# Performance work log

Measured on AMD Instinct MI355X. Metric: run time of the kernel, lower is better.

Reference implementation:

```python
import jax, jax.numpy as jnp
import numpy as np

B = 131072
D = 64
H1 = 512
H2 = 256
NC = 128  # nurse classes
DC = 128  # doctor classes
EPS = 1e-5
NEG = -1e9


def _kaiming(key, fan_in, fan_out):
    # kaiming_normal_ with mode='fan_out', relu gain: std = sqrt(2/fan_out)
    return jax.random.normal(key, (fan_in, fan_out), jnp.float32) * jnp.sqrt(2.0 / fan_out)


def setup_inputs() -> dict:
    key = jax.random.key(0)
    ks = jax.random.split(key, 16)
    x = jax.random.normal(ks[0], (B, D), jnp.float32)
    sn = jax.random.randint(ks[1], (B,), 0, NC)
    sd = jax.random.randint(ks[2], (B,), 0, DC)
    # last-4 / last-3 columns carry the per-sample max class thresholds
    x = x.at[:, -4].set(sn.astype(jnp.float32)).at[:, -3].set(sd.astype(jnp.float32))
    inp = {
        'x': x,
        'W0': _kaiming(ks[3], D, H1), 'b0': jnp.zeros((H1,), jnp.float32),
        'g0': jnp.ones((H1,), jnp.float32), 'be0': jnp.zeros((H1,), jnp.float32),
        'rm0': jax.random.normal(ks[4], (H1,), jnp.float32) * 0.1,
        'rv0': jax.random.uniform(ks[5], (H1,), jnp.float32, 0.5, 1.5),
        'W1': _kaiming(ks[6], H1, H2), 'b1': jnp.zeros((H2,), jnp.float32),
        'g1': jnp.ones((H2,), jnp.float32), 'be1': jnp.zeros((H2,), jnp.float32),
        'rm1': jax.random.normal(ks[7], (H2,), jnp.float32) * 0.1,
        'rv1': jax.random.uniform(ks[8], (H2,), jnp.float32, 0.5, 1.5),
        'nW1': _kaiming(ks[9], H2, 64), 'nb1': jnp.zeros((64,), jnp.float32),
        'nW2': _kaiming(ks[10], 64, NC), 'nb2': jnp.zeros((NC,), jnp.float32),
        'dW1': _kaiming(ks[11], H2, 64), 'db1': jnp.zeros((64,), jnp.float32),
        'dW2': _kaiming(ks[12], 64, DC), 'db2': jnp.zeros((DC,), jnp.float32),
    }
    return inp


def _bn(h, g, be, rm, rv):
    # BatchNorm1d inference: normalize with running stats
    return (h - rm) * (g * jax.lax.rsqrt(rv + EPS)) + be


def reference(x, W0, b0, g0, be0, rm0, rv0, W1, b1, g1, be1, rm1, rv1,
              nW1, nb1, nW2, nb2, dW1, db1, dW2, db2):
    s_nurse = x[:, -4].astype(jnp.int32)   # [B]
    s_doctor = x[:, -3].astype(jnp.int32)  # [B]

    h = jax.nn.relu(_bn(x @ W0 + b0, g0, be0, rm0, rv0))   # [B,H1]
    h = jax.nn.relu(_bn(h @ W1 + b1, g1, be1, rm1, rv1))   # [B,H2]

    nurse_logits = jax.nn.relu(h @ nW1 + nb1) @ nW2 + nb2   # [B,NC]
    doctor_logits = jax.nn.relu(h @ dW1 + db1) @ dW2 + db2  # [B,DC]

    # vectorized range mask: positions <= s_max are kept
    nmask = (jnp.arange(NC)[None, :] <= s_nurse[:, None]).astype(nurse_logits.dtype)
    dmask = (jnp.arange(DC)[None, :] <= s_doctor[:, None]).astype(doctor_logits.dtype)
    nurse_logits = nurse_logits * nmask + (1.0 - nmask) * NEG
    doctor_logits = doctor_logits * dmask + (1.0 - dmask) * NEG
    return (nurse_logits, doctor_logits)
```

## Files before the change

kernel.cpp:

```cpp
#include <hip/hip_runtime.h>

#define NB 131072
#define NEG9 -1e9f

typedef __attribute__((ext_vector_type(8))) __bf16 bf16x8;
typedef __attribute__((ext_vector_type(4))) float f32x4;
typedef __attribute__((ext_vector_type(2))) unsigned int u32x2;
typedef __attribute__((ext_vector_type(4))) unsigned int u32x4;

__device__ __forceinline__ f32x4 mfma16(bf16x8 a, bf16x8 b, f32x4 c) {
    return __builtin_amdgcn_mfma_f32_16x16x32_bf16(a, b, c, 0, 0, 0);
}

__device__ __forceinline__ unsigned pk(float h, float l) {
    return __builtin_amdgcn_perm(__builtin_bit_cast(unsigned, h),
                                 __builtin_bit_cast(unsigned, l), 0x07060302u);
}
__device__ __forceinline__ unsigned pku(unsigned h, unsigned l) {
    return __builtin_amdgcn_perm(h, l, 0x07060302u);
}

__device__ __forceinline__ unsigned short f2bf(float f) {
    unsigned u = __builtin_bit_cast(unsigned, f);
    u += 0x7fffu + ((u >> 16) & 1u);
    return (unsigned short)(u >> 16);
}

struct __align__(16) Wspace {
    unsigned short W0t[512][64];
    unsigned short W1t[256][512];
    unsigned short nW1t[64][256];
    unsigned short dW1t[64][256];
    unsigned short nW2t[128][64];
    unsigned short dW2t[128][64];
    float c0[512];
    float c1[256];
    float nb1c[64], db1c[64];
    float nb2c[128], db2c[128];
};

__device__ Wspace g_ws;

__global__ __launch_bounds__(256) void prep_kernel(
    const float* __restrict__ W0, const float* __restrict__ b0,
    const float* __restrict__ g0, const float* __restrict__ be0,
    const float* __restrict__ rm0, const float* __restrict__ rv0,
    const float* __restrict__ W1, const float* __restrict__ b1,
    const float* __restrict__ g1, const float* __restrict__ be1,
    const float* __restrict__ rm1, const float* __restrict__ rv1,
    const float* __restrict__ nW1, const float* __restrict__ nb1,
    const float* __restrict__ nW2, const float* __restrict__ nb2,
    const float* __restrict__ dW1, const float* __restrict__ db1,
    const float* __restrict__ dW2, const float* __restrict__ db2)
{
    const int b = blockIdx.x;
    const int t = threadIdx.x;

    if (b == 52) {
        {
            int i = t;          g_ws.c0[i] = (b0[i] - rm0[i]) * (g0[i] * rsqrtf(rv0[i] + 1e-5f)) + be0[i];
            i = t + 256;        g_ws.c0[i] = (b0[i] - rm0[i]) * (g0[i] * rsqrtf(rv0[i] + 1e-5f)) + be0[i];
        }
        g_ws.c1[t] = (b1[t] - rm1[t]) * (g1[t] * rsqrtf(rv1[t] + 1e-5f)) + be1[t];
        if (t < 64)  { g_ws.nb1c[t] = nb1[t]; g_ws.db1c[t] = db1[t]; }
        if (t < 128) { g_ws.nb2c[t] = nb2[t]; g_ws.db2c[t] = db2[t]; }
        return;
    }

    const float* src; unsigned short* dst;
    const float* gp = nullptr; const float* rvp = nullptr;
    int sld, dld, k0, n0;
    if (b < 32)      { src = W1;  dst = (unsigned short*)g_ws.W1t;  sld = 256; dld = 512;
                       k0 = (b >> 2) * 64; n0 = (b & 3) * 64; gp = g1; rvp = rv1; }
    else if (b < 40) { src = W0;  dst = (unsigned short*)g_ws.W0t;  sld = 512; dld = 64;
                       k0 = 0; n0 = (b - 32) * 64; gp = g0; rvp = rv0; }
    else if (b < 44) { src = nW1; dst = (unsigned short*)g_ws.nW1t; sld = 64;  dld = 256;
                       k0 = (b - 40) * 64; n0 = 0; }
    else if (b < 48) { src = dW1; dst = (unsigned short*)g_ws.dW1t; sld = 64;  dld = 256;
                       k0 = (b - 44) * 64; n0 = 0; }
    else if (b < 50) { src = nW2; dst = (unsigned short*)g_ws.nW2t; sld = 128; dld = 64;
                       k0 = 0; n0 = (b - 48) * 64; }
    else             { src = dW2; dst = (unsigned short*)g_ws.dW2t; sld = 128; dld = 64;
                       k0 = 0; n0 = (b - 50) * 64; }

    __shared__ unsigned short tile[64][66];

    const int rr = t >> 4;
    const int cc = (t & 15) * 4;

#pragma unroll
    for (int g = 0; g < 4; ++g) {
        const int r = rr + g * 16;
        f32x4 v = *(const f32x4*)&src[(size_t)(k0 + r) * sld + n0 + cc];
        if (gp) {
            f32x4 gv = *(const f32x4*)&gp[n0 + cc];
            f32x4 rv = *(const f32x4*)&rvp[n0 + cc];
            v[0] *= gv[0] * rsqrtf(rv[0] + 1e-5f);
            v[1] *= gv[1] * rsqrtf(rv[1] + 1e-5f);
            v[2] *= gv[2] * rsqrtf(rv[2] + 1e-5f);
            v[3] *= gv[3] * rsqrtf(rv[3] + 1e-5f);
        }
        *(unsigned*)&tile[r][cc]     = (unsigned)f2bf(v[0]) | ((unsigned)f2bf(v[1]) << 16);
        *(unsigned*)&tile[r][cc + 2] = (unsigned)f2bf(v[2]) | ((unsigned)f2bf(v[3]) << 16);
    }
    __syncthreads();

#pragma unroll
    for (int g = 0; g < 4; ++g) {
        const int n = rr + g * 16;
        unsigned o01 = (unsigned)tile[cc + 0][n] | ((unsigned)tile[cc + 1][n] << 16);
        unsigned o23 = (unsigned)tile[cc + 2][n] | ((unsigned)tile[cc + 3][n] << 16);
        u32x2 o = { o01, o23 };
        *(u32x2*)&dst[(size_t)(n0 + n) * dld + k0 + cc] = o;
    }
}

__global__ __launch_bounds__(512, 4) void fused_mlp(
    const u32x4* __restrict__ xu, float* __restrict__ out)
{
    __shared__ __align__(16) unsigned short sXs[8 * 64 * 8];
    __shared__ __align__(16) unsigned short sH0[64 * 64 * 8];

    const int tid = threadIdx.x;
    const int w = tid >> 6;
    const int lane = tid & 63;
    const int m = lane & 15;
    const int q = lane >> 4;
    const int qh = q >> 1;
    const int ql = (q & 1) * 4;
    const int row0 = blockIdx.x * 64;

    {
        int r = tid >> 3, g = tid & 7;
        u32x4 v0 = __builtin_nontemporal_load(&xu[(size_t)(row0 + r) * 16 + g * 2]);
        u32x4 v1 = __builtin_nontemporal_load(&xu[(size_t)(row0 + r) * 16 + g * 2 + 1]);
        u32x4 p = { pku(v0[1], v0[0]), pku(v0[3], v0[2]), pku(v1[1], v1[0]), pku(v1[3], v1[2]) };
        *(u32x4*)&sXs[(g * 64 + r) * 8] = p;
    }
    __syncthreads();

    bf16x8 xr[2][4];
#pragma unroll
    for (int g2 = 0; g2 < 2; ++g2)
#pragma unroll
        for (int mt = 0; mt < 4; ++mt)
            xr[g2][mt] = *(const bf16x8*)&sXs[((g2 * 4 + q) * 64 + mt * 16 + m) * 8];

#pragma unroll
    for (int nt = 0; nt < 4; ++nt) {
        const int gcb = w * 64 + nt * 16;
        bf16x8 wa0 = *(const bf16x8*)&g_ws.W0t[gcb + m][q * 8];
        bf16x8 wa1 = *(const bf16x8*)&g_ws.W0t[gcb + m][32 + q * 8];
        f32x4 bias = *(const f32x4*)&g_ws.c0[gcb + q * 4];
        const int kg = w * 8 + nt * 2 + qh;
#pragma unroll
        for (int mt = 0; mt < 4; ++mt) {
            f32x4 c = {0.f, 0.f, 0.f, 0.f};
            c = mfma16(wa0, xr[0][mt], c);
            c = mfma16(wa1, xr[1][mt], c);
            u32x2 pw = { pk(fmaxf(c[1] + bias[1], 0.f), fmaxf(c[0] + bias[0], 0.f)),
                         pk(fmaxf(c[3] + bias[3], 0.f), fmaxf(c[2] + bias[2], 0.f)) };
            *(u32x2*)&sH0[(kg * 64 + mt * 16 + m) * 8 + ql] = pw;
        }
    }
    __syncthreads();

    f32x4 acc1[2][4];
#pragma unroll
    for (int a = 0; a < 2; ++a)
#pragma unroll
        for (int b = 0; b < 4; ++b) acc1[a][b] = f32x4{0.f, 0.f, 0.f, 0.f};

#pragma unroll
    for (int ks = 0; ks < 16; ++ks) {
        bf16x8 wb[2], ab[4];
#pragma unroll
        for (int nt = 0; nt < 2; ++nt)
            wb[nt] = *(const bf16x8*)&g_ws.W1t[w * 32 + nt * 16 + m][ks * 32 + q * 8];
#pragma unroll
        for (int mt = 0; mt < 4; ++mt)
            ab[mt] = *(const bf16x8*)&sH0[((ks * 4 + q) * 64 + mt * 16 + m) * 8];
#pragma unroll
        for (int nt = 0; nt < 2; ++nt)
#pragma unroll
            for (int mt = 0; mt < 4; ++mt)
                acc1[nt][mt] = mfma16(wb[nt], ab[mt], acc1[nt][mt]);
    }
    __syncthreads();

#pragma unroll
    for (int nt = 0; nt < 2; ++nt) {
        const int cb = w * 32 + nt * 16;
        f32x4 bias = *(const f32x4*)&g_ws.c1[cb + q * 4];
        const int kg = w * 4 + nt * 2 + qh;
#pragma unroll
        for (int mt = 0; mt < 4; ++mt) {
            f32x4 c = acc1[nt][mt];
            u32x2 pw = { pk(fmaxf(c[1] + bias[1], 0.f), fmaxf(c[0] + bias[0], 0.f)),
                         pk(fmaxf(c[3] + bias[3], 0.f), fmaxf(c[2] + bias[2], 0.f)) };
            *(u32x2*)&sH0[(kg * 64 + mt * 16 + m) * 8 + ql] = pw;
        }
    }
    __syncthreads();

    const int head = w >> 2;
    {
        const int cb = (w & 3) * 16;
        const unsigned short (*Wh)[256] = head ? g_ws.dW1t : g_ws.nW1t;
        const float* bh = head ? g_ws.db1c : g_ws.nb1c;
        f32x4 acc[4];
#pragma unroll
        for (int b = 0; b < 4; ++b) acc[b] = f32x4{0.f, 0.f, 0.f, 0.f};
#pragma unroll
        for (int ks = 0; ks < 8; ++ks) {
            bf16x8 wh = *(const bf16x8*)&Wh[cb + m][ks * 32 + q * 8];
#pragma unroll
            for (int mt = 0; mt < 4; ++mt) {
                bf16x8 ab = *(const bf16x8*)&sH0[((ks * 4 + q) * 64 + mt * 16 + m) * 8];
                acc[mt] = mfma16(wh, ab, acc[mt]);
            }
        }
        __syncthreads();
        unsigned short* Ah = sH0 + (head ? 4096 : 0);
        f32x4 bias = *(const f32x4*)&bh[cb + q * 4];
        const int kg = (w & 3) * 2 + qh;
#pragma unroll
        for (int mt = 0; mt < 4; ++mt) {
            f32x4 c = acc[mt];
            u32x2 pw = { pk(fmaxf(c[1] + bias[1], 0.f), fmaxf(c[0] + bias[0], 0.f)),
                         pk(fmaxf(c[3] + bias[3], 0.f), fmaxf(c[2] + bias[2], 0.f)) };
            *(u32x2*)&Ah[(kg * 64 + mt * 16 + m) * 8 + ql] = pw;
        }
    }
    __syncthreads();

    {
        const unsigned short (*W2)[64] = head ? g_ws.dW2t : g_ws.nW2t;
        const float* b2 = head ? g_ws.db2c : g_ws.nb2c;
        const unsigned short* Ah = sH0 + (head ? 4096 : 0);
        float* op = out + (size_t)head * (size_t)NB * 128;

        int thr[4];
#pragma unroll
        for (int mt = 0; mt < 4; ++mt) {
            unsigned tv = *(const unsigned*)&sXs[(7 * 64 + mt * 16 + m) * 8 + 4];
            thr[mt] = (int)__builtin_bit_cast(float, head ? (tv & 0xffff0000u) : (tv << 16));
        }
#pragma unroll
        for (int ct = 0; ct < 2; ++ct) {
            const int ocb = (w & 3) * 32 + ct * 16;
            bf16x8 w0 = *(const bf16x8*)&W2[ocb + m][q * 8];
            bf16x8 w1 = *(const bf16x8*)&W2[ocb + m][32 + q * 8];
            f32x4 bias = *(const f32x4*)&b2[ocb + q * 4];
#pragma unroll
            for (int mt = 0; mt < 4; ++mt) {
                bf16x8 a0 = *(const bf16x8*)&Ah[(q * 64 + mt * 16 + m) * 8];
                bf16x8 a1 = *(const bf16x8*)&Ah[((4 + q) * 64 + mt * 16 + m) * 8];
                f32x4 c = {0.f, 0.f, 0.f, 0.f};
                c = mfma16(w0, a0, c);
                c = mfma16(w1, a1, c);
                const int ci = ocb + q * 4;
                const int t = thr[mt];
                f32x4 v;
                v[0] = (ci + 0 <= t) ? c[0] + bias[0] : NEG9;
                v[1] = (ci + 1 <= t) ? c[1] + bias[1] : NEG9;
                v[2] = (ci + 2 <= t) ? c[2] + bias[2] : NEG9;
                v[3] = (ci + 3 <= t) ? c[3] + bias[3] : NEG9;
                *(f32x4*)&op[(size_t)(row0 + mt * 16 + m) * 128 + ci] = v;
            }
        }
    }
}

extern "C" void kernel_launch(void* const* d_in, const int* in_sizes, int n_in,
                              void* d_out, int out_size, void* d_ws, size_t ws_size,
                              hipStream_t stream) {
    (void)in_sizes; (void)n_in; (void)d_ws; (void)ws_size;

    prep_kernel<<<53, 256, 0, stream>>>(
        (const float*)d_in[1], (const float*)d_in[2], (const float*)d_in[3],
        (const float*)d_in[4], (const float*)d_in[5], (const float*)d_in[6],
        (const float*)d_in[7], (const float*)d_in[8], (const float*)d_in[9],
        (const float*)d_in[10], (const float*)d_in[11], (const float*)d_in[12],
        (const float*)d_in[13], (const float*)d_in[14], (const float*)d_in[15],
        (const float*)d_in[16], (const float*)d_in[17], (const float*)d_in[18],
        (const float*)d_in[19], (const float*)d_in[20]);

    fused_mlp<<<NB / 64, 512, 0, stream>>>((const u32x4*)d_in[0], (float*)d_out);
}
```

Baseline: 285.8 us.

## Use 4 waves per 64-row block, each computing wider output tiles

The fused MLP kernel drops from 8 wavefronts to 4 wavefronts per 64-row block. Each wave now computes twice as many output columns in every layer. This reuses each loaded activation fragment across more MFMAs and halves the redundant shared-memory reads of the A operand. The cost is more accumulator registers per wave and fewer waves to hide latency (launch bounds 256,2), which risks lower occupancy or register spills.

```diff
diff --git a/kernel.cpp b/kernel.cpp
--- a/kernel.cpp
+++ b/kernel.cpp
@@ -115,7 +115,7 @@
     }
 }
 
-__global__ __launch_bounds__(512, 4) void fused_mlp(
+__global__ __launch_bounds__(256, 2) void fused_mlp(
     const u32x4* __restrict__ xu, float* __restrict__ out)
 {
     __shared__ __align__(16) unsigned short sXs[8 * 64 * 8];
@@ -132,10 +132,14 @@
 
     {
         int r = tid >> 3, g = tid & 7;
-        u32x4 v0 = __builtin_nontemporal_load(&xu[(size_t)(row0 + r) * 16 + g * 2]);
-        u32x4 v1 = __builtin_nontemporal_load(&xu[(size_t)(row0 + r) * 16 + g * 2 + 1]);
-        u32x4 p = { pku(v0[1], v0[0]), pku(v0[3], v0[2]), pku(v1[1], v1[0]), pku(v1[3], v1[2]) };
-        *(u32x4*)&sXs[(g * 64 + r) * 8] = p;
+#pragma unroll
+        for (int hh = 0; hh < 2; ++hh) {
+            int rr = r + hh * 32;
+            u32x4 v0 = __builtin_nontemporal_load(&xu[(size_t)(row0 + rr) * 16 + g * 2]);
+            u32x4 v1 = __builtin_nontemporal_load(&xu[(size_t)(row0 + rr) * 16 + g * 2 + 1]);
+            u32x4 p = { pku(v0[1], v0[0]), pku(v0[3], v0[2]), pku(v1[1], v1[0]), pku(v1[3], v1[2]) };
+            *(u32x4*)&sXs[(g * 64 + rr) * 8] = p;
+        }
     }
     __syncthreads();
 
@@ -147,12 +151,12 @@
             xr[g2][mt] = *(const bf16x8*)&sXs[((g2 * 4 + q) * 64 + mt * 16 + m) * 8];
 
 #pragma unroll
-    for (int nt = 0; nt < 4; ++nt) {
-        const int gcb = w * 64 + nt * 16;
+    for (int nt = 0; nt < 8; ++nt) {
+        const int gcb = w * 128 + nt * 16;
         bf16x8 wa0 = *(const bf16x8*)&g_ws.W0t[gcb + m][q * 8];
         bf16x8 wa1 = *(const bf16x8*)&g_ws.W0t[gcb + m][32 + q * 8];
         f32x4 bias = *(const f32x4*)&g_ws.c0[gcb + q * 4];
-        const int kg = w * 8 + nt * 2 + qh;
+        const int kg = w * 16 + nt * 2 + qh;
 #pragma unroll
         for (int mt = 0; mt < 4; ++mt) {
             f32x4 c = {0.f, 0.f, 0.f, 0.f};
@@ -165,23 +169,23 @@
     }
     __syncthreads();
 
-    f32x4 acc1[2][4];
-#pragma unroll
-    for (int a = 0; a < 2; ++a)
+    f32x4 acc1[4][4];
+#pragma unroll
+    for (int a = 0; a < 4; ++a)
 #pragma unroll
         for (int b = 0; b < 4; ++b) acc1[a][b] = f32x4{0.f, 0.f, 0.f, 0.f};
 
 #pragma unroll
     for (int ks = 0; ks < 16; ++ks) {
-        bf16x8 wb[2], ab[4];
-#pragma unroll
-        for (int nt = 0; nt < 2; ++nt)
-            wb[nt] = *(const bf16x8*)&g_ws.W1t[w * 32 + nt * 16 + m][ks * 32 + q * 8];
+        bf16x8 wb[4], ab[4];
+#pragma unroll
+        for (int nt = 0; nt < 4; ++nt)
+            wb[nt] = *(const bf16x8*)&g_ws.W1t[w * 64 + nt * 16 + m][ks * 32 + q * 8];
 #pragma unroll
         for (int mt = 0; mt < 4; ++mt)
             ab[mt] = *(const bf16x8*)&sH0[((ks * 4 + q) * 64 + mt * 16 + m) * 8];
 #pragma unroll
-        for (int nt = 0; nt < 2; ++nt)
+        for (int nt = 0; nt < 4; ++nt)
 #pragma unroll
             for (int mt = 0; mt < 4; ++mt)
                 acc1[nt][mt] = mfma16(wb[nt], ab[mt], acc1[nt][mt]);
@@ -189,10 +193,10 @@
     __syncthreads();
 
 #pragma unroll
-    for (int nt = 0; nt < 2; ++nt) {
-        const int cb = w * 32 + nt * 16;
+    for (int nt = 0; nt < 4; ++nt) {
+        const int cb = w * 64 + nt * 16;
         f32x4 bias = *(const f32x4*)&g_ws.c1[cb + q * 4];
-        const int kg = w * 4 + nt * 2 + qh;
+        const int kg = w * 8 + nt * 2 + qh;
 #pragma unroll
         for (int mt = 0; mt < 4; ++mt) {
             f32x4 c = acc1[nt][mt];
@@ -203,33 +207,44 @@
     }
     __syncthreads();
 
-    const int head = w >> 2;
+    const int head = w >> 1;
+    const int hw = w & 1;
     {
-        const int cb = (w & 3) * 16;
         const unsigned short (*Wh)[256] = head ? g_ws.dW1t : g_ws.nW1t;
         const float* bh = head ? g_ws.db1c : g_ws.nb1c;
-        f32x4 acc[4];
-#pragma unroll
-        for (int b = 0; b < 4; ++b) acc[b] = f32x4{0.f, 0.f, 0.f, 0.f};
+        f32x4 acc[2][4];
+#pragma unroll
+        for (int a = 0; a < 2; ++a)
+#pragma unroll
+            for (int b = 0; b < 4; ++b) acc[a][b] = f32x4{0.f, 0.f, 0.f, 0.f};
 #pragma unroll
         for (int ks = 0; ks < 8; ++ks) {
-            bf16x8 wh = *(const bf16x8*)&Wh[cb + m][ks * 32 + q * 8];
-#pragma unroll
-            for (int mt = 0; mt < 4; ++mt) {
-                bf16x8 ab = *(const bf16x8*)&sH0[((ks * 4 + q) * 64 + mt * 16 + m) * 8];
-                acc[mt] = mfma16(wh, ab, acc[mt]);
-            }
+            bf16x8 wh[2], ab[4];
+#pragma unroll
+            for (int nt = 0; nt < 2; ++nt)
+                wh[nt] = *(const bf16x8*)&Wh[hw * 32 + nt * 16 + m][ks * 32 + q * 8];
+#pragma unroll
+            for (int mt = 0; mt < 4; ++mt)
+                ab[mt] = *(const bf16x8*)&sH0[((ks * 4 + q) * 64 + mt * 16 + m) * 8];
+#pragma unroll
+            for (int nt = 0; nt < 2; ++nt)
+#pragma unroll
+                for (int mt = 0; mt < 4; ++mt)
+                    acc[nt][mt] = mfma16(wh[nt], ab[mt], acc[nt][mt]);
         }
         __syncthreads();
         unsigned short* Ah = sH0 + (head ? 4096 : 0);
-        f32x4 bias = *(const f32x4*)&bh[cb + q * 4];
-        const int kg = (w & 3) * 2 + qh;
-#pragma unroll
-        for (int mt = 0; mt < 4; ++mt) {
-            f32x4 c = acc[mt];
-            u32x2 pw = { pk(fmaxf(c[1] + bias[1], 0.f), fmaxf(c[0] + bias[0], 0.f)),
-                         pk(fmaxf(c[3] + bias[3], 0.f), fmaxf(c[2] + bias[2], 0.f)) };
-            *(u32x2*)&Ah[(kg * 64 + mt * 16 + m) * 8 + ql] = pw;
+#pragma unroll
+        for (int nt = 0; nt < 2; ++nt) {
+            f32x4 bias = *(const f32x4*)&bh[hw * 32 + nt * 16 + q * 4];
+            const int kg = hw * 4 + nt * 2 + qh;
+#pragma unroll
+            for (int mt = 0; mt < 4; ++mt) {
+                f32x4 c = acc[nt][mt];
+                u32x2 pw = { pk(fmaxf(c[1] + bias[1], 0.f), fmaxf(c[0] + bias[0], 0.f)),
+                             pk(fmaxf(c[3] + bias[3], 0.f), fmaxf(c[2] + bias[2], 0.f)) };
+                *(u32x2*)&Ah[(kg * 64 + mt * 16 + m) * 8 + ql] = pw;
+            }
         }
     }
     __syncthreads();
@@ -247,8 +262,8 @@
             thr[mt] = (int)__builtin_bit_cast(float, head ? (tv & 0xffff0000u) : (tv << 16));
         }
 #pragma unroll
-        for (int ct = 0; ct < 2; ++ct) {
-            const int ocb = (w & 3) * 32 + ct * 16;
+        for (int ct = 0; ct < 4; ++ct) {
+            const int ocb = hw * 64 + ct * 16;
             bf16x8 w0 = *(const bf16x8*)&W2[ocb + m][q * 8];
             bf16x8 w1 = *(const bf16x8*)&W2[ocb + m][32 + q * 8];
             f32x4 bias = *(const f32x4*)&b2[ocb + q * 4];
@@ -286,5 +301,5 @@
         (const float*)d_in[16], (const float*)d_in[17], (const float*)d_in[18],
         (const float*)d_in[19], (const float*)d_in[20]);
 
-    fused_mlp<<<NB / 64, 512, 0, stream>>>((const u32x4*)d_in[0], (float*)d_out);
-}
+    fused_mlp<<<NB / 64, 256, 0, stream>>>((const u32x4*)d_in[0], (float*)d_out);
+}
```

After: 290.7 us. About the same (+1.7%).

## Split 64-row tile into two 32-row halves and software-pipeline layers across them

Applied to the files above, without the earlier changes.

Splits each block's 64 rows into halves A and B with separate LDS buffers, staggering the stages so one half's layer computation overlaps the other half's layer work (for example, layer 0 of B is interleaved into the layer-1 loop of A). This is meant to hide the barrier and LDS round-trip stalls between dependent layers by giving the MFMA units independent work. It adds extra syncthreads and reloads of the weights per half, since each weight fragment is now fetched twice.

```diff
diff --git a/kernel.cpp b/kernel.cpp
--- a/kernel.cpp
+++ b/kernel.cpp
@@ -119,7 +119,7 @@
     const u32x4* __restrict__ xu, float* __restrict__ out)
 {
     __shared__ __align__(16) unsigned short sXs[8 * 64 * 8];
-    __shared__ __align__(16) unsigned short sH0[64 * 64 * 8];
+    __shared__ __align__(16) unsigned short sH0[2 * 64 * 32 * 8];
 
     const int tid = threadIdx.x;
     const int w = tid >> 6;
@@ -130,6 +130,9 @@
     const int ql = (q & 1) * 4;
     const int row0 = blockIdx.x * 64;
 
+    unsigned short* const sA = sH0;
+    unsigned short* const sB = sH0 + 16384;
+
     {
         int r = tid >> 3, g = tid & 7;
         u32x4 v0 = __builtin_nontemporal_load(&xu[(size_t)(row0 + r) * 16 + g * 2]);
@@ -139,52 +142,79 @@
     }
     __syncthreads();
 
-    bf16x8 xr[2][4];
-#pragma unroll
-    for (int g2 = 0; g2 < 2; ++g2)
-#pragma unroll
-        for (int mt = 0; mt < 4; ++mt)
-            xr[g2][mt] = *(const bf16x8*)&sXs[((g2 * 4 + q) * 64 + mt * 16 + m) * 8];
-
-#pragma unroll
-    for (int nt = 0; nt < 4; ++nt) {
-        const int gcb = w * 64 + nt * 16;
-        bf16x8 wa0 = *(const bf16x8*)&g_ws.W0t[gcb + m][q * 8];
-        bf16x8 wa1 = *(const bf16x8*)&g_ws.W0t[gcb + m][32 + q * 8];
-        f32x4 bias = *(const f32x4*)&g_ws.c0[gcb + q * 4];
-        const int kg = w * 8 + nt * 2 + qh;
-#pragma unroll
-        for (int mt = 0; mt < 4; ++mt) {
-            f32x4 c = {0.f, 0.f, 0.f, 0.f};
-            c = mfma16(wa0, xr[0][mt], c);
-            c = mfma16(wa1, xr[1][mt], c);
-            u32x2 pw = { pk(fmaxf(c[1] + bias[1], 0.f), fmaxf(c[0] + bias[0], 0.f)),
-                         pk(fmaxf(c[3] + bias[3], 0.f), fmaxf(c[2] + bias[2], 0.f)) };
-            *(u32x2*)&sH0[(kg * 64 + mt * 16 + m) * 8 + ql] = pw;
-        }
-    }
-    __syncthreads();
-
-    f32x4 acc1[2][4];
+    const int head = w >> 2;
+
+    {
+        bf16x8 xrA[2][2];
+#pragma unroll
+        for (int g2 = 0; g2 < 2; ++g2)
+#pragma unroll
+            for (int mt = 0; mt < 2; ++mt)
+                xrA[g2][mt] = *(const bf16x8*)&sXs[((g2 * 4 + q) * 64 + mt * 16 + m) * 8];
+#pragma unroll
+        for (int nt = 0; nt < 4; ++nt) {
+            const int gcb = w * 64 + nt * 16;
+            bf16x8 wa0 = *(const bf16x8*)&g_ws.W0t[gcb + m][q * 8];
+            bf16x8 wa1 = *(const bf16x8*)&g_ws.W0t[gcb + m][32 + q * 8];
+            f32x4 bias = *(const f32x4*)&g_ws.c0[gcb + q * 4];
+            const int kg = w * 8 + nt * 2 + qh;
+#pragma unroll
+            for (int mt = 0; mt < 2; ++mt) {
+                f32x4 c = {0.f, 0.f, 0.f, 0.f};
+                c = mfma16(wa0, xrA[0][mt], c);
+                c = mfma16(wa1, xrA[1][mt], c);
+                u32x2 pw = { pk(fmaxf(c[1] + bias[1], 0.f), fmaxf(c[0] + bias[0], 0.f)),
+                             pk(fmaxf(c[3] + bias[3], 0.f), fmaxf(c[2] + bias[2], 0.f)) };
+                *(u32x2*)&sA[(kg * 32 + mt * 16 + m) * 8 + ql] = pw;
+            }
+        }
+    }
+    __syncthreads();
+
+    f32x4 acc1A[2][2];
 #pragma unroll
     for (int a = 0; a < 2; ++a)
 #pragma unroll
-        for (int b = 0; b < 4; ++b) acc1[a][b] = f32x4{0.f, 0.f, 0.f, 0.f};
-
-#pragma unroll
-    for (int ks = 0; ks < 16; ++ks) {
-        bf16x8 wb[2], ab[4];
-#pragma unroll
-        for (int nt = 0; nt < 2; ++nt)
-            wb[nt] = *(const bf16x8*)&g_ws.W1t[w * 32 + nt * 16 + m][ks * 32 + q * 8];
-#pragma unroll
-        for (int mt = 0; mt < 4; ++mt)
-            ab[mt] = *(const bf16x8*)&sH0[((ks * 4 + q) * 64 + mt * 16 + m) * 8];
-#pragma unroll
-        for (int nt = 0; nt < 2; ++nt)
-#pragma unroll
-            for (int mt = 0; mt < 4; ++mt)
-                acc1[nt][mt] = mfma16(wb[nt], ab[mt], acc1[nt][mt]);
+        for (int b = 0; b < 2; ++b) acc1A[a][b] = f32x4{0.f, 0.f, 0.f, 0.f};
+    {
+        bf16x8 xrB[2][2];
+#pragma unroll
+        for (int g2 = 0; g2 < 2; ++g2)
+#pragma unroll
+            for (int mt = 0; mt < 2; ++mt)
+                xrB[g2][mt] = *(const bf16x8*)&sXs[((g2 * 4 + q) * 64 + 32 + mt * 16 + m) * 8];
+#pragma unroll
+        for (int ks = 0; ks < 16; ++ks) {
+            bf16x8 wb[2], ab[2];
+#pragma unroll
+            for (int nt = 0; nt < 2; ++nt)
+                wb[nt] = *(const bf16x8*)&g_ws.W1t[w * 32 + nt * 16 + m][ks * 32 + q * 8];
+#pragma unroll
+            for (int mt = 0; mt < 2; ++mt)
+                ab[mt] = *(const bf16x8*)&sA[((ks * 4 + q) * 32 + mt * 16 + m) * 8];
+#pragma unroll
+            for (int nt = 0; nt < 2; ++nt)
+#pragma unroll
+                for (int mt = 0; mt < 2; ++mt)
+                    acc1A[nt][mt] = mfma16(wb[nt], ab[mt], acc1A[nt][mt]);
+            if ((ks & 3) == 0) {
+                const int nt2 = ks >> 2;
+                const int gcb = w * 64 + nt2 * 16;
+                bf16x8 wa0 = *(const bf16x8*)&g_ws.W0t[gcb + m][q * 8];
+                bf16x8 wa1 = *(const bf16x8*)&g_ws.W0t[gcb + m][32 + q * 8];
+                f32x4 bias = *(const f32x4*)&g_ws.c0[gcb + q * 4];
+                const int kg = w * 8 + nt2 * 2 + qh;
+#pragma unroll
+                for (int mt = 0; mt < 2; ++mt) {
+                    f32x4 c = {0.f, 0.f, 0.f, 0.f};
+                    c = mfma16(wa0, xrB[0][mt], c);
+                    c = mfma16(wa1, xrB[1][mt], c);
+                    u32x2 pw = { pk(fmaxf(c[1] + bias[1], 0.f), fmaxf(c[0] + bias[0], 0.f)),
+                                 pk(fmaxf(c[3] + bias[3], 0.f), fmaxf(c[2] + bias[2], 0.f)) };
+                    *(u32x2*)&sB[(kg * 32 + mt * 16 + m) * 8 + ql] = pw;
+                }
+            }
+        }
     }
     __syncthreads();
 
@@ -194,55 +224,110 @@
         f32x4 bias = *(const f32x4*)&g_ws.c1[cb + q * 4];
         const int kg = w * 4 + nt * 2 + qh;
 #pragma unroll
-        for (int mt = 0; mt < 4; ++mt) {
-            f32x4 c = acc1[nt][mt];
+        for (int mt = 0; mt < 2; ++mt) {
+            f32x4 c = acc1A[nt][mt];
             u32x2 pw = { pk(fmaxf(c[1] + bias[1], 0.f), fmaxf(c[0] + bias[0], 0.f)),
                          pk(fmaxf(c[3] + bias[3], 0.f), fmaxf(c[2] + bias[2], 0.f)) };
-            *(u32x2*)&sH0[(kg * 64 + mt * 16 + m) * 8 + ql] = pw;
-        }
-    }
-    __syncthreads();
-
-    const int head = w >> 2;
-    {
-        const int cb = (w & 3) * 16;
-        const unsigned short (*Wh)[256] = head ? g_ws.dW1t : g_ws.nW1t;
-        const float* bh = head ? g_ws.db1c : g_ws.nb1c;
-        f32x4 acc[4];
-#pragma unroll
-        for (int b = 0; b < 4; ++b) acc[b] = f32x4{0.f, 0.f, 0.f, 0.f};
-#pragma unroll
-        for (int ks = 0; ks < 8; ++ks) {
-            bf16x8 wh = *(const bf16x8*)&Wh[cb + m][ks * 32 + q * 8];
-#pragma unroll
-            for (int mt = 0; mt < 4; ++mt) {
-                bf16x8 ab = *(const bf16x8*)&sH0[((ks * 4 + q) * 64 + mt * 16 + m) * 8];
-                acc[mt] = mfma16(wh, ab, acc[mt]);
-            }
-        }
-        __syncthreads();
-        unsigned short* Ah = sH0 + (head ? 4096 : 0);
-        f32x4 bias = *(const f32x4*)&bh[cb + q * 4];
-        const int kg = (w & 3) * 2 + qh;
-#pragma unroll
-        for (int mt = 0; mt < 4; ++mt) {
-            f32x4 c = acc[mt];
+            *(u32x2*)&sA[(kg * 32 + mt * 16 + m) * 8 + ql] = pw;
+        }
+    }
+    f32x4 acc1B[2][2];
+#pragma unroll
+    for (int a = 0; a < 2; ++a)
+#pragma unroll
+        for (int b = 0; b < 2; ++b) acc1B[a][b] = f32x4{0.f, 0.f, 0.f, 0.f};
+#pragma unroll
+    for (int ks = 0; ks < 16; ++ks) {
+        bf16x8 wb[2], ab[2];
+#pragma unroll
+        for (int nt = 0; nt < 2; ++nt)
+            wb[nt] = *(const bf16x8*)&g_ws.W1t[w * 32 + nt * 16 + m][ks * 32 + q * 8];
+#pragma unroll
+        for (int mt = 0; mt < 2; ++mt)
+            ab[mt] = *(const bf16x8*)&sB[((ks * 4 + q) * 32 + mt * 16 + m) * 8];
+#pragma unroll
+        for (int nt = 0; nt < 2; ++nt)
+#pragma unroll
+            for (int mt = 0; mt < 2; ++mt)
+                acc1B[nt][mt] = mfma16(wb[nt], ab[mt], acc1B[nt][mt]);
+    }
+    __syncthreads();
+
+#pragma unroll
+    for (int nt = 0; nt < 2; ++nt) {
+        const int cb = w * 32 + nt * 16;
+        f32x4 bias = *(const f32x4*)&g_ws.c1[cb + q * 4];
+        const int kg = w * 4 + nt * 2 + qh;
+#pragma unroll
+        for (int mt = 0; mt < 2; ++mt) {
+            f32x4 c = acc1B[nt][mt];
             u32x2 pw = { pk(fmaxf(c[1] + bias[1], 0.f), fmaxf(c[0] + bias[0], 0.f)),
                          pk(fmaxf(c[3] + bias[3], 0.f), fmaxf(c[2] + bias[2], 0.f)) };
-            *(u32x2*)&Ah[(kg * 64 + mt * 16 + m) * 8 + ql] = pw;
-        }
-    }
-    __syncthreads();
-
-    {
-        const unsigned short (*W2)[64] = head ? g_ws.dW2t : g_ws.nW2t;
-        const float* b2 = head ? g_ws.db2c : g_ws.nb2c;
-        const unsigned short* Ah = sH0 + (head ? 4096 : 0);
-        float* op = out + (size_t)head * (size_t)NB * 128;
-
-        int thr[4];
-#pragma unroll
-        for (int mt = 0; mt < 4; ++mt) {
+            *(u32x2*)&sB[(kg * 32 + mt * 16 + m) * 8 + ql] = pw;
+        }
+    }
+    const int cb1 = (w & 3) * 16;
+    const unsigned short (*Wh)[256] = head ? g_ws.dW1t : g_ws.nW1t;
+    const float* bh = head ? g_ws.db1c : g_ws.nb1c;
+    f32x4 ahA[2];
+    ahA[0] = f32x4{0.f, 0.f, 0.f, 0.f}; ahA[1] = f32x4{0.f, 0.f, 0.f, 0.f};
+#pragma unroll
+    for (int ks = 0; ks < 8; ++ks) {
+        bf16x8 wh = *(const bf16x8*)&Wh[cb1 + m][ks * 32 + q * 8];
+#pragma unroll
+        for (int mt = 0; mt < 2; ++mt) {
+            bf16x8 ab = *(const bf16x8*)&sA[((ks * 4 + q) * 32 + mt * 16 + m) * 8];
+            ahA[mt] = mfma16(wh, ab, ahA[mt]);
+        }
+    }
+    __syncthreads();
+
+    {
+        unsigned short* AhA = sA + 8192 + head * 2048;
+        f32x4 bias = *(const f32x4*)&bh[cb1 + q * 4];
+        const int kg = (w & 3) * 2 + qh;
+#pragma unroll
+        for (int mt = 0; mt < 2; ++mt) {
+            f32x4 c = ahA[mt];
+            u32x2 pw = { pk(fmaxf(c[1] + bias[1], 0.f), fmaxf(c[0] + bias[0], 0.f)),
+                         pk(fmaxf(c[3] + bias[3], 0.f), fmaxf(c[2] + bias[2], 0.f)) };
+            *(u32x2*)&AhA[(kg * 32 + mt * 16 + m) * 8 + ql] = pw;
+        }
+    }
+    f32x4 ahB[2];
+    ahB[0] = f32x4{0.f, 0.f, 0.f, 0.f}; ahB[1] = f32x4{0.f, 0.f, 0.f, 0.f};
+#pragma unroll
+    for (int ks = 0; ks < 8; ++ks) {
+        bf16x8 wh = *(const bf16x8*)&Wh[cb1 + m][ks * 32 + q * 8];
+#pragma unroll
+        for (int mt = 0; mt < 2; ++mt) {
+            bf16x8 ab = *(const bf16x8*)&sB[((ks * 4 + q) * 32 + mt * 16 + m) * 8];
+            ahB[mt] = mfma16(wh, ab, ahB[mt]);
+        }
+    }
+    __syncthreads();
+
+    const unsigned short (*W2)[64] = head ? g_ws.dW2t : g_ws.nW2t;
+    const float* b2 = head ? g_ws.db2c : g_ws.nb2c;
+    float* op = out + (size_t)head * (size_t)NB * 128;
+
+    {
+        unsigned short* AhB = sB + 8192 + head * 2048;
+        f32x4 bias = *(const f32x4*)&bh[cb1 + q * 4];
+        const int kg = (w & 3) * 2 + qh;
+#pragma unroll
+        for (int mt = 0; mt < 2; ++mt) {
+            f32x4 c = ahB[mt];
+            u32x2 pw = { pk(fmaxf(c[1] + bias[1], 0.f), fmaxf(c[0] + bias[0], 0.f)),
+                         pk(fmaxf(c[3] + bias[3], 0.f), fmaxf(c[2] + bias[2], 0.f)) };
+            *(u32x2*)&AhB[(kg * 32 + mt * 16 + m) * 8 + ql] = pw;
+        }
+    }
+    {
+        const unsigned short* AhA = sA + 8192 + head * 2048;
+        int thr[2];
+#pragma unroll
+        for (int mt = 0; mt < 2; ++mt) {
             unsigned tv = *(const unsigned*)&sXs[(7 * 64 + mt * 16 + m) * 8 + 4];
             thr[mt] = (int)__builtin_bit_cast(float, head ? (tv & 0xffff0000u) : (tv << 16));
         }
@@ -253,9 +338,9 @@
             bf16x8 w1 = *(const bf16x8*)&W2[ocb + m][32 + q * 8];
             f32x4 bias = *(const f32x4*)&b2[ocb + q * 4];
 #pragma unroll
-            for (int mt = 0; mt < 4; ++mt) {
-                bf16x8 a0 = *(const bf16x8*)&Ah[(q * 64 + mt * 16 + m) * 8];
-                bf16x8 a1 = *(const bf16x8*)&Ah[((4 + q) * 64 + mt * 16 + m) * 8];
+            for (int mt = 0; mt < 2; ++mt) {
+                bf16x8 a0 = *(const bf16x8*)&AhA[(q * 32 + mt * 16 + m) * 8];
+                bf16x8 a1 = *(const bf16x8*)&AhA[((4 + q) * 32 + mt * 16 + m) * 8];
                 f32x4 c = {0.f, 0.f, 0.f, 0.f};
                 c = mfma16(w0, a0, c);
                 c = mfma16(w1, a1, c);
@@ -270,6 +355,40 @@
             }
         }
     }
+    __syncthreads();
+
+    {
+        const unsigned short* AhB = sB + 8192 + head * 2048;
+        int thr[2];
+#pragma unroll
+        for (int mt = 0; mt < 2; ++mt) {
+            unsigned tv = *(const unsigned*)&sXs[(7 * 64 + 32 + mt * 16 + m) * 8 + 4];
+            thr[mt] = (int)__builtin_bit_cast(float, head ? (tv & 0xffff0000u) : (tv << 16));
+        }
+#pragma unroll
+        for (int ct = 0; ct < 2; ++ct) {
+            const int ocb = (w & 3) * 32 + ct * 16;
+            bf16x8 w0 = *(const bf16x8*)&W2[ocb + m][q * 8];
+            bf16x8 w1 = *(const bf16x8*)&W2[ocb + m][32 + q * 8];
+            f32x4 bias = *(const f32x4*)&b2[ocb + q * 4];
+#pragma unroll
+            for (int mt = 0; mt < 2; ++mt) {
+                bf16x8 a0 = *(const bf16x8*)&AhB[(q * 32 + mt * 16 + m) * 8];
+                bf16x8 a1 = *(const bf16x8*)&AhB[((4 + q) * 32 + mt * 16 + m) * 8];
+                f32x4 c = {0.f, 0.f, 0.f, 0.f};
+                c = mfma16(w0, a0, c);
+                c = mfma16(w1, a1, c);
+                const int ci = ocb + q * 4;
+                const int t = thr[mt];
+                f32x4 v;
+                v[0] = (ci + 0 <= t) ? c[0] + bias[0] : NEG9;
+                v[1] = (ci + 1 <= t) ? c[1] + bias[1] : NEG9;
+                v[2] = (ci + 2 <= t) ? c[2] + bias[2] : NEG9;
+                v[3] = (ci + 3 <= t) ? c[3] + bias[3] : NEG9;
+                *(f32x4*)&op[(size_t)(row0 + 32 + mt * 16 + m) * 128 + ci] = v;
+            }
+        }
+    }
 }
 
 extern "C" void kernel_launch(void* const* d_in, const int* in_sizes, int n_in,
```

Result: slower. 382.2 us (+33.7%).

## Process 128 rows per block and split layer-0 hidden into two chunks

Applied to the files above, without the earlier changes.

Doubles the per-block row tile from 64 to 128 so every weight fragment loaded from global memory is reused across twice as many MFMAs. To keep LDS use bounded, the 512-wide first hidden layer is now computed in two 256-column chunks, each consumed right away by the second-layer accumulation. This interleaves layers 0 and 1 with extra barriers. It doubles the accumulator registers (acc1 is now 2x8 tiles), which could reduce occupancy under the 512x4 launch bounds or cause spills, and it halves the grid size.

```diff
diff --git a/kernel.cpp b/kernel.cpp
--- a/kernel.cpp
+++ b/kernel.cpp
@@ -118,8 +118,8 @@
 __global__ __launch_bounds__(512, 4) void fused_mlp(
     const u32x4* __restrict__ xu, float* __restrict__ out)
 {
-    __shared__ __align__(16) unsigned short sXs[8 * 64 * 8];
-    __shared__ __align__(16) unsigned short sH0[64 * 64 * 8];
+    __shared__ __align__(16) unsigned short sXs[8 * 128 * 8];
+    __shared__ __align__(16) unsigned short sH[32 * 128 * 8];
 
     const int tid = threadIdx.x;
     const int w = tid >> 6;
@@ -128,65 +128,66 @@
     const int q = lane >> 4;
     const int qh = q >> 1;
     const int ql = (q & 1) * 4;
-    const int row0 = blockIdx.x * 64;
+    const int row0 = blockIdx.x * 128;
 
     {
         int r = tid >> 3, g = tid & 7;
-        u32x4 v0 = __builtin_nontemporal_load(&xu[(size_t)(row0 + r) * 16 + g * 2]);
-        u32x4 v1 = __builtin_nontemporal_load(&xu[(size_t)(row0 + r) * 16 + g * 2 + 1]);
-        u32x4 p = { pku(v0[1], v0[0]), pku(v0[3], v0[2]), pku(v1[1], v1[0]), pku(v1[3], v1[2]) };
-        *(u32x4*)&sXs[(g * 64 + r) * 8] = p;
-    }
-    __syncthreads();
-
-    bf16x8 xr[2][4];
-#pragma unroll
-    for (int g2 = 0; g2 < 2; ++g2)
-#pragma unroll
-        for (int mt = 0; mt < 4; ++mt)
-            xr[g2][mt] = *(const bf16x8*)&sXs[((g2 * 4 + q) * 64 + mt * 16 + m) * 8];
-
-#pragma unroll
-    for (int nt = 0; nt < 4; ++nt) {
-        const int gcb = w * 64 + nt * 16;
-        bf16x8 wa0 = *(const bf16x8*)&g_ws.W0t[gcb + m][q * 8];
-        bf16x8 wa1 = *(const bf16x8*)&g_ws.W0t[gcb + m][32 + q * 8];
-        f32x4 bias = *(const f32x4*)&g_ws.c0[gcb + q * 4];
-        const int kg = w * 8 + nt * 2 + qh;
-#pragma unroll
-        for (int mt = 0; mt < 4; ++mt) {
-            f32x4 c = {0.f, 0.f, 0.f, 0.f};
-            c = mfma16(wa0, xr[0][mt], c);
-            c = mfma16(wa1, xr[1][mt], c);
-            u32x2 pw = { pk(fmaxf(c[1] + bias[1], 0.f), fmaxf(c[0] + bias[0], 0.f)),
-                         pk(fmaxf(c[3] + bias[3], 0.f), fmaxf(c[2] + bias[2], 0.f)) };
-            *(u32x2*)&sH0[(kg * 64 + mt * 16 + m) * 8 + ql] = pw;
-        }
-    }
-    __syncthreads();
-
-    f32x4 acc1[2][4];
+#pragma unroll
+        for (int hh = 0; hh < 2; ++hh) {
+            int rr = r + hh * 64;
+            u32x4 v0 = __builtin_nontemporal_load(&xu[(size_t)(row0 + rr) * 16 + g * 2]);
+            u32x4 v1 = __builtin_nontemporal_load(&xu[(size_t)(row0 + rr) * 16 + g * 2 + 1]);
+            u32x4 p = { pku(v0[1], v0[0]), pku(v0[3], v0[2]), pku(v1[1], v1[0]), pku(v1[3], v1[2]) };
+            *(u32x4*)&sXs[(g * 128 + rr) * 8] = p;
+        }
+    }
+    __syncthreads();
+
+    f32x4 acc1[2][8];
 #pragma unroll
     for (int a = 0; a < 2; ++a)
 #pragma unroll
-        for (int b = 0; b < 4; ++b) acc1[a][b] = f32x4{0.f, 0.f, 0.f, 0.f};
-
-#pragma unroll
-    for (int ks = 0; ks < 16; ++ks) {
-        bf16x8 wb[2], ab[4];
-#pragma unroll
-        for (int nt = 0; nt < 2; ++nt)
-            wb[nt] = *(const bf16x8*)&g_ws.W1t[w * 32 + nt * 16 + m][ks * 32 + q * 8];
-#pragma unroll
-        for (int mt = 0; mt < 4; ++mt)
-            ab[mt] = *(const bf16x8*)&sH0[((ks * 4 + q) * 64 + mt * 16 + m) * 8];
-#pragma unroll
-        for (int nt = 0; nt < 2; ++nt)
-#pragma unroll
-            for (int mt = 0; mt < 4; ++mt)
-                acc1[nt][mt] = mfma16(wb[nt], ab[mt], acc1[nt][mt]);
-    }
-    __syncthreads();
+        for (int b = 0; b < 8; ++b) acc1[a][b] = f32x4{0.f, 0.f, 0.f, 0.f};
+
+    for (int ch = 0; ch < 2; ++ch) {
+#pragma unroll
+        for (int nt = 0; nt < 2; ++nt) {
+            const int gcb = ch * 256 + w * 32 + nt * 16;
+            bf16x8 wa0 = *(const bf16x8*)&g_ws.W0t[gcb + m][q * 8];
+            bf16x8 wa1 = *(const bf16x8*)&g_ws.W0t[gcb + m][32 + q * 8];
+            f32x4 bias = *(const f32x4*)&g_ws.c0[gcb + q * 4];
+            const int kg = w * 4 + nt * 2 + qh;
+#pragma unroll
+            for (int mt = 0; mt < 8; ++mt) {
+                bf16x8 xq0 = *(const bf16x8*)&sXs[(q * 128 + mt * 16 + m) * 8];
+                bf16x8 xq1 = *(const bf16x8*)&sXs[((4 + q) * 128 + mt * 16 + m) * 8];
+                f32x4 c = {0.f, 0.f, 0.f, 0.f};
+                c = mfma16(wa0, xq0, c);
+                c = mfma16(wa1, xq1, c);
+                u32x2 pw = { pk(fmaxf(c[1] + bias[1], 0.f), fmaxf(c[0] + bias[0], 0.f)),
+                             pk(fmaxf(c[3] + bias[3], 0.f), fmaxf(c[2] + bias[2], 0.f)) };
+                *(u32x2*)&sH[(kg * 128 + mt * 16 + m) * 8 + ql] = pw;
+            }
+        }
+        __syncthreads();
+
+#pragma unroll
+        for (int ks = 0; ks < 8; ++ks) {
+            bf16x8 wb[2], ab[8];
+#pragma unroll
+            for (int nt = 0; nt < 2; ++nt)
+                wb[nt] = *(const bf16x8*)&g_ws.W1t[w * 32 + nt * 16 + m][ch * 256 + ks * 32 + q * 8];
+#pragma unroll
+            for (int mt = 0; mt < 8; ++mt)
+                ab[mt] = *(const bf16x8*)&sH[((ks * 4 + q) * 128 + mt * 16 + m) * 8];
+#pragma unroll
+            for (int nt = 0; nt < 2; ++nt)
+#pragma unroll
+                for (int mt = 0; mt < 8; ++mt)
+                    acc1[nt][mt] = mfma16(wb[nt], ab[mt], acc1[nt][mt]);
+        }
+        __syncthreads();
+    }
 
 #pragma unroll
     for (int nt = 0; nt < 2; ++nt) {
@@ -194,11 +195,11 @@
         f32x4 bias = *(const f32x4*)&g_ws.c1[cb + q * 4];
         const int kg = w * 4 + nt * 2 + qh;
 #pragma unroll
-        for (int mt = 0; mt < 4; ++mt) {
+        for (int mt = 0; mt < 8; ++mt) {
             f32x4 c = acc1[nt][mt];
             u32x2 pw = { pk(fmaxf(c[1] + bias[1], 0.f), fmaxf(c[0] + bias[0], 0.f)),
                          pk(fmaxf(c[3] + bias[3], 0.f), fmaxf(c[2] + bias[2], 0.f)) };
-            *(u32x2*)&sH0[(kg * 64 + mt * 16 + m) * 8 + ql] = pw;
+            *(u32x2*)&sH[(kg * 128 + mt * 16 + m) * 8 + ql] = pw;
         }
     }
     __syncthreads();
@@ -208,28 +209,28 @@
         const int cb = (w & 3) * 16;
         const unsigned short (*Wh)[256] = head ? g_ws.dW1t : g_ws.nW1t;
         const float* bh = head ? g_ws.db1c : g_ws.nb1c;
-        f32x4 acc[4];
-#pragma unroll
-        for (int b = 0; b < 4; ++b) acc[b] = f32x4{0.f, 0.f, 0.f, 0.f};
+        f32x4 acc[8];
+#pragma unroll
+        for (int b = 0; b < 8; ++b) acc[b] = f32x4{0.f, 0.f, 0.f, 0.f};
 #pragma unroll
         for (int ks = 0; ks < 8; ++ks) {
             bf16x8 wh = *(const bf16x8*)&Wh[cb + m][ks * 32 + q * 8];
 #pragma unroll
-            for (int mt = 0; mt < 4; ++mt) {
-                bf16x8 ab = *(const bf16x8*)&sH0[((ks * 4 + q) * 64 + mt * 16 + m) * 8];
+            for (int mt = 0; mt < 8; ++mt) {
+                bf16x8 ab = *(const bf16x8*)&sH[((ks * 4 + q) * 128 + mt * 16 + m) * 8];
                 acc[mt] = mfma16(wh, ab, acc[mt]);
             }
         }
         __syncthreads();
-        unsigned short* Ah = sH0 + (head ? 4096 : 0);
+        unsigned short* Ah = sH + head * 8192;
         f32x4 bias = *(const f32x4*)&bh[cb + q * 4];
         const int kg = (w & 3) * 2 + qh;
 #pragma unroll
-        for (int mt = 0; mt < 4; ++mt) {
+        for (int mt = 0; mt < 8; ++mt) {
             f32x4 c = acc[mt];
             u32x2 pw = { pk(fmaxf(c[1] + bias[1], 0.f), fmaxf(c[0] + bias[0], 0.f)),
                          pk(fmaxf(c[3] + bias[3], 0.f), fmaxf(c[2] + bias[2], 0.f)) };
-            *(u32x2*)&Ah[(kg * 64 + mt * 16 + m) * 8 + ql] = pw;
+            *(u32x2*)&Ah[(kg * 128 + mt * 16 + m) * 8 + ql] = pw;
         }
     }
     __syncthreads();
@@ -237,13 +238,13 @@
     {
         const unsigned short (*W2)[64] = head ? g_ws.dW2t : g_ws.nW2t;
         const float* b2 = head ? g_ws.db2c : g_ws.nb2c;
-        const unsigned short* Ah = sH0 + (head ? 4096 : 0);
+        const unsigned short* Ah = sH + head * 8192;
         float* op = out + (size_t)head * (size_t)NB * 128;
 
-        int thr[4];
-#pragma unroll
-        for (int mt = 0; mt < 4; ++mt) {
-            unsigned tv = *(const unsigned*)&sXs[(7 * 64 + mt * 16 + m) * 8 + 4];
+        int thr[8];
+#pragma unroll
+        for (int mt = 0; mt < 8; ++mt) {
+            unsigned tv = *(const unsigned*)&sXs[(7 * 128 + mt * 16 + m) * 8 + 4];
             thr[mt] = (int)__builtin_bit_cast(float, head ? (tv & 0xffff0000u) : (tv << 16));
         }
 #pragma unroll
@@ -253,9 +254,9 @@
             bf16x8 w1 = *(const bf16x8*)&W2[ocb + m][32 + q * 8];
             f32x4 bias = *(const f32x4*)&b2[ocb + q * 4];
 #pragma unroll
-            for (int mt = 0; mt < 4; ++mt) {
-                bf16x8 a0 = *(const bf16x8*)&Ah[(q * 64 + mt * 16 + m) * 8];
-                bf16x8 a1 = *(const bf16x8*)&Ah[((4 + q) * 64 + mt * 16 + m) * 8];
+            for (int mt = 0; mt < 8; ++mt) {
+                bf16x8 a0 = *(const bf16x8*)&Ah[(q * 128 + mt * 16 + m) * 8];
+                bf16x8 a1 = *(const bf16x8*)&Ah[((4 + q) * 128 + mt * 16 + m) * 8];
                 f32x4 c = {0.f, 0.f, 0.f, 0.f};
                 c = mfma16(w0, a0, c);
                 c = mfma16(w1, a1, c);
@@ -286,5 +287,5 @@
         (const float*)d_in[16], (const float*)d_in[17], (const float*)d_in[18],
         (const float*)d_in[19], (const float*)d_in[20]);
 
-    fused_mlp<<<NB / 64, 512, 0, stream>>>((const u32x4*)d_in[0], (float*)d_out);
-}
+    fused_mlp<<<NB / 128, 512, 0, stream>>>((const u32x4*)d_in[0], (float*)d_out);
+}
```

Measured after the change: 275.1 us. -3.7%, faster.
